# Performance work log

Measured on AMD Instinct MI355X. Metric: run time of the kernel, lower is better.

The kernel has to match this reference:

```python
import jax, jax.numpy as jnp
import numpy as np


def _topk_axis(x, k, axis, largest):
    # lax.top_k works on the last axis, largest, sorted descending.
    xm = jnp.moveaxis(x, axis, -1)
    if largest:
        vals, idx = jax.lax.top_k(xm, k)
    else:
        vals, idx = jax.lax.top_k(-xm, k)
        vals = -vals  # ascending smallest-k, matching torch.topk(largest=False, sorted=True)
    return jnp.moveaxis(vals, -1, axis), jnp.moveaxis(idx, -1, axis)


def setup_inputs() -> dict:
    key = jax.random.key(0)
    k0, k1, k2 = jax.random.split(key, 3)
    v_0 = jax.random.normal(k0, (4096, 32000), dtype=jnp.float32)
    v_1 = jax.random.normal(k1, (8, 16, 64, 4096), dtype=jnp.float32)
    v_2 = jax.random.normal(k2, (100000, 512), dtype=jnp.float32)
    return {"v_0": v_0, "v_1": v_1, "v_2": v_2}


def reference(v_0, v_1, v_2):
    # TopK_0: k=2, dim=1, largest, sorted
    v_4, v_5 = _topk_axis(v_0, 2, 1, largest=True)
    # TopK_1: k=4, dim=3, smallest, sorted
    v_7, v_8 = _topk_axis(v_1, 4, 3, largest=False)
    # TopK_2: k=3, dim=0, largest, sorted
    v_10, v_11 = _topk_axis(v_2, 3, 0, largest=True)
    return (v_4, v_5, v_7, v_8, v_10, v_11)
```

## Files before the change

kernel.cpp:

```cpp
#include <hip/hip_runtime.h>
#include <limits.h>
#include <math.h>

typedef unsigned long long u64;
typedef unsigned int u32;

__device__ __forceinline__ u32 f2ord(float v) {
    u32 u = __float_as_uint(v);
    return (u & 0x80000000u) ? ~u : (u | 0x80000000u);
}
__device__ __forceinline__ float ord2f(u32 s) {
    u32 u = (s & 0x80000000u) ? (s & 0x7FFFFFFFu) : ~s;
    return __uint_as_float(u);
}
__device__ __forceinline__ u64 keylg(float v, u32 i) { return ((u64)f2ord(v) << 32) | (u64)(~i); }
__device__ __forceinline__ u64 keysm(float v, u32 i) { return ((u64)f2ord(v) << 32) | (u64)i; }
__device__ __forceinline__ float val_of(u64 k) { return ord2f((u32)(k >> 32)); }
__device__ __forceinline__ float idxf_lg(u64 k) { return (float)(~(u32)k); }
__device__ __forceinline__ float idxf_sm(u64 k) { return (float)((u32)k); }

__device__ __forceinline__ u64 mx64(u64 a, u64 b) { return a > b ? a : b; }
__device__ __forceinline__ u64 mn64(u64 a, u64 b) { return a < b ? a : b; }

__device__ __forceinline__ void ins2_lg(u64& s0, u64& s1, u64 k) {
    u64 t0 = mx64(s0, k), r0 = mn64(s0, k);
    s0 = t0; s1 = mx64(s1, r0);
}
__device__ __forceinline__ void ins3_lg(u64& s0, u64& s1, u64& s2, u64 k) {
    u64 t0 = mx64(s0, k), r0 = mn64(s0, k);
    u64 t1 = mx64(s1, r0), r1 = mn64(s1, r0);
    s0 = t0; s1 = t1; s2 = mx64(s2, r1);
}
__device__ __forceinline__ void ins4_sm(u64& s0, u64& s1, u64& s2, u64& s3, u64 k) {
    u64 t0 = mn64(s0, k), r0 = mx64(s0, k);
    u64 t1 = mn64(s1, r0), r1 = mx64(s1, r0);
    u64 t2 = mn64(s2, r1), r2 = mx64(s2, r1);
    s0 = t0; s1 = t1; s2 = t2; s3 = mn64(s3, r2);
}

__device__ __forceinline__ void ce_max(u64& a, u64& b) { u64 h = mx64(a, b), l = mn64(a, b); a = h; b = l; }
__device__ __forceinline__ void ce_min(u64& a, u64& b) { u64 l = mn64(a, b), h = mx64(a, b); a = l; b = h; }

__device__ __forceinline__ void merge2_lg(u64& a0, u64& a1, u64 b0, u64 b1) {
    u64 l0 = mx64(a0, b1), l1 = mx64(a1, b0);
    a0 = mx64(l0, l1); a1 = mn64(l0, l1);
}
__device__ __forceinline__ void merge3_lg(u64& a0, u64& a1, u64& a2, u64 b0, u64 b1, u64 b2) {
    u64 l0 = mx64(a0, b2), l1 = mx64(a1, b1), l2 = mx64(a2, b0);
    ce_max(l0, l1); ce_max(l1, l2); ce_max(l0, l1);
    a0 = l0; a1 = l1; a2 = l2;
}
__device__ __forceinline__ void merge4_sm(u64& a0, u64& a1, u64& a2, u64& a3,
                                          u64 b0, u64 b1, u64 b2, u64 b3) {
    u64 l0 = mn64(a0, b3), l1 = mn64(a1, b2), l2 = mn64(a2, b1), l3 = mn64(a3, b0);
    ce_min(l0, l2); ce_min(l1, l3); ce_min(l0, l1); ce_min(l2, l3);
    a0 = l0; a1 = l1; a2 = l2; a3 = l3;
}

__device__ __forceinline__ u64 shx64(u64 v, int m) {
    u32 hi = __shfl_xor((u32)(v >> 32), m);
    u32 lo = __shfl_xor((u32)v, m);
    return ((u64)hi << 32) | (u64)lo;
}

__global__ __launch_bounds__(256) void mega_kernel(
    const float* __restrict__ x0, float* __restrict__ o0v, float* __restrict__ o0i,
    const float* __restrict__ x1, float* __restrict__ o1v, float* __restrict__ o1i,
    const float* __restrict__ x2, u64* __restrict__ part, int rpb)
{
    const int bid  = blockIdx.x;
    const int wave = threadIdx.x >> 6;
    const int lane = threadIdx.x & 63;

    if (bid < 1024) {
        const int row = bid * 4 + wave;
        const float4* xr = (const float4*)(x0 + (size_t)row * 32000);
        u64 s0 = 0, s1 = 0;

#define K0UPD(f, b) \
        ins2_lg(s0, s1, keylg((f).x, (u32)(b)));     \
        ins2_lg(s0, s1, keylg((f).y, (u32)(b) + 1)); \
        ins2_lg(s0, s1, keylg((f).z, (u32)(b) + 2)); \
        ins2_lg(s0, s1, keylg((f).w, (u32)(b) + 3))

        int v = lane;
        for (int it = 0; it < 31; ++it, v += 256) {
            float4 t0 = xr[v];
            float4 t1 = xr[v + 64];
            float4 t2 = xr[v + 128];
            float4 t3 = xr[v + 192];
            K0UPD(t0, v * 4); K0UPD(t1, (v + 64) * 4);
            K0UPD(t2, (v + 128) * 4); K0UPD(t3, (v + 192) * 4);
        }
        { float4 t = xr[v]; K0UPD(t, v * 4); }
#undef K0UPD

        for (int m = 1; m < 64; m <<= 1) {
            u64 b0 = shx64(s0, m), b1 = shx64(s1, m);
            merge2_lg(s0, s1, b0, b1);
        }
        if (lane == 0) {
            o0v[row * 2 + 0] = val_of(s0);  o0v[row * 2 + 1] = val_of(s1);
            o0i[row * 2 + 0] = idxf_lg(s0); o0i[row * 2 + 1] = idxf_lg(s1);
        }

    } else if (bid < 3072) {
        const int row = (bid - 1024) * 4 + wave;
        const float4* xr = (const float4*)(x1 + (size_t)row * 4096);
        u64 s0 = ~0ull, s1 = ~0ull, s2 = ~0ull, s3 = ~0ull;

#define K1UPD(f, b) \
        ins4_sm(s0, s1, s2, s3, keysm((f).x, (u32)(b)));     \
        ins4_sm(s0, s1, s2, s3, keysm((f).y, (u32)(b) + 1)); \
        ins4_sm(s0, s1, s2, s3, keysm((f).z, (u32)(b) + 2)); \
        ins4_sm(s0, s1, s2, s3, keysm((f).w, (u32)(b) + 3))

        int v = lane;
        for (int it = 0; it < 4; ++it, v += 256) {
            float4 t0 = xr[v];
            float4 t1 = xr[v + 64];
            float4 t2 = xr[v + 128];
            float4 t3 = xr[v + 192];
            K1UPD(t0, v * 4); K1UPD(t1, (v + 64) * 4);
            K1UPD(t2, (v + 128) * 4); K1UPD(t3, (v + 192) * 4);
        }
#undef K1UPD

        for (int m = 1; m < 64; m <<= 1) {
            u64 b0 = shx64(s0, m), b1 = shx64(s1, m);
            u64 b2 = shx64(s2, m), b3 = shx64(s3, m);
            merge4_sm(s0, s1, s2, s3, b0, b1, b2, b3);
        }
        if (lane == 0) {
            o1v[row * 4 + 0] = val_of(s0);  o1v[row * 4 + 1] = val_of(s1);
            o1v[row * 4 + 2] = val_of(s2);  o1v[row * 4 + 3] = val_of(s3);
            o1i[row * 4 + 0] = idxf_sm(s0); o1i[row * 4 + 1] = idxf_sm(s1);
            o1i[row * 4 + 2] = idxf_sm(s2); o1i[row * 4 + 3] = idxf_sm(s3);
        }

    } else {
        const int blk = bid - 3072;
        const int t   = threadIdx.x;
        const int h   = t >> 7;
        const int c0  = (t & 127) * 4;
        int rbeg = blk * rpb;
        int rend = rbeg + rpb; if (rend > 100000) rend = 100000;

        u64 a[4][3];
#pragma unroll
        for (int c = 0; c < 4; ++c) { a[c][0] = 0; a[c][1] = 0; a[c][2] = 0; }

#define P1LOAD(r) (*(const float4*)(x2 + (size_t)(r) * 512 + c0))
#define P1UPD(f, rr) \
        ins3_lg(a[0][0], a[0][1], a[0][2], keylg((f).x, (u32)(rr))); \
        ins3_lg(a[1][0], a[1][1], a[1][2], keylg((f).y, (u32)(rr))); \
        ins3_lg(a[2][0], a[2][1], a[2][2], keylg((f).z, (u32)(rr))); \
        ins3_lg(a[3][0], a[3][1], a[3][2], keylg((f).w, (u32)(rr)))

        int r = rbeg + h;
        for (; r + 6 < rend; r += 8) {
            float4 f0 = P1LOAD(r);
            float4 f1 = P1LOAD(r + 2);
            float4 f2 = P1LOAD(r + 4);
            float4 f3 = P1LOAD(r + 6);
            P1UPD(f0, r); P1UPD(f1, r + 2); P1UPD(f2, r + 4); P1UPD(f3, r + 6);
        }
        for (; r < rend; r += 2) {
            float4 f0 = P1LOAD(r);
            P1UPD(f0, r);
        }
#undef P1LOAD
#undef P1UPD

        const int p = blk * 2 + h;
        u64* base = part + (size_t)p * 3 * 512;
#pragma unroll
        for (int k = 0; k < 3; ++k)
#pragma unroll
            for (int c = 0; c < 4; ++c)
                base[k * 512 + c0 + c] = a[c][k];
    }
}

__global__ __launch_bounds__(256) void topk2_p2a(
    const u64* __restrict__ part, u64* __restrict__ part2)
{
    const int b = blockIdx.x;
    const int s = b >> 1, cb = b & 1;
    const int col = cb * 256 + threadIdx.x;

    u64 a0 = 0, a1 = 0, a2 = 0;
    const u64* base = part + (size_t)s * 8 * 1536;
#pragma unroll
    for (int p = 0; p < 8; ++p) {
        const u64* q = base + (size_t)p * 1536;
        u64 x0 = q[col], x1 = q[512 + col], x2 = q[1024 + col];
        merge3_lg(a0, a1, a2, x0, x1, x2);
    }
    part2[((size_t)s * 3 + 0) * 512 + col] = a0;
    part2[((size_t)s * 3 + 1) * 512 + col] = a1;
    part2[((size_t)s * 3 + 2) * 512 + col] = a2;
}

__global__ __launch_bounds__(256) void topk2_p2b(
    const u64* __restrict__ part2, float* __restrict__ outv, float* __restrict__ outi)
{
    const int wave = threadIdx.x >> 6;
    const int lane = threadIdx.x & 63;
    const int col  = blockIdx.x * 4 + wave;

    const u64* q0 = part2 + (size_t)lane * 1536 + col;
    const u64* q1 = part2 + (size_t)(lane + 64) * 1536 + col;
    u64 a0 = q0[0], a1 = q0[512], a2 = q0[1024];
    merge3_lg(a0, a1, a2, q1[0], q1[512], q1[1024]);

    for (int m = 1; m < 64; m <<= 1) {
        u64 b0 = shx64(a0, m), b1 = shx64(a1, m), b2 = shx64(a2, m);
        merge3_lg(a0, a1, a2, b0, b1, b2);
    }

    if (lane == 0) {
        outv[0 * 512 + col] = val_of(a0);
        outv[1 * 512 + col] = val_of(a1);
        outv[2 * 512 + col] = val_of(a2);
        outi[0 * 512 + col] = idxf_lg(a0);
        outi[1 * 512 + col] = idxf_lg(a1);
        outi[2 * 512 + col] = idxf_lg(a2);
    }
}

__global__ __launch_bounds__(256) void topk2_direct(
    const float* __restrict__ x, float* __restrict__ outv, float* __restrict__ outi)
{
    const int col = blockIdx.x * 256 + threadIdx.x;
    u64 a0 = 0, a1 = 0, a2 = 0;
    for (int r = 0; r < 100000; ++r) {
        float v = x[(size_t)r * 512 + col];
        ins3_lg(a0, a1, a2, keylg(v, (u32)r));
    }
    outv[0 * 512 + col] = val_of(a0);
    outv[1 * 512 + col] = val_of(a1);
    outv[2 * 512 + col] = val_of(a2);
    outi[0 * 512 + col] = idxf_lg(a0);
    outi[1 * 512 + col] = idxf_lg(a1);
    outi[2 * 512 + col] = idxf_lg(a2);
}

__global__ __launch_bounds__(256) void noop_kernel() {}

extern "C" void kernel_launch(void* const* d_in, const int* in_sizes, int n_in,
                              void* d_out, int out_size, void* d_ws, size_t ws_size,
                              hipStream_t stream) {
    const float* v0 = (const float*)d_in[0];
    const float* v1 = (const float*)d_in[1];
    const float* v2 = (const float*)d_in[2];
    float* out = (float*)d_out;

    float* o_v4  = out;
    float* o_v5  = out + 8192;
    float* o_v7  = out + 16384;
    float* o_v8  = out + 49152;
    float* o_v10 = out + 81920;
    float* o_v11 = out + 83456;

    const int NB = 512;
    int rpb = (100000 + NB - 1) / NB;
    if (rpb & 1) rpb++;
    size_t need = ((size_t)NB * 2 + 128) * 3 * 512 * sizeof(u64);

    if (ws_size >= need) {
        u64* part  = (u64*)d_ws;
        u64* part2 = part + (size_t)NB * 2 * 3 * 512;
        mega_kernel<<<3584, 256, 0, stream>>>(v0, o_v4, o_v5,
                                              v1, o_v7, o_v8,
                                              v2, part, rpb);
        topk2_p2a<<<256, 256, 0, stream>>>(part, part2);
        topk2_p2b<<<128, 256, 0, stream>>>(part2, o_v10, o_v11);
    } else {
        mega_kernel<<<3072, 256, 0, stream>>>(v0, o_v4, o_v5,
                                              v1, o_v7, o_v8,
                                              v2, (u64*)d_ws, 1 << 30);
        topk2_direct<<<2, 256, 0, stream>>>(v2, o_v10, o_v11);
    }
}
```

Measured before the change: 190.2 us.

## Schedule column-topk blocks first and collapse two-stage reduction into one kernel

The column-wise top-3 partial blocks move to the front of the mega-kernel grid, so the long per-column scans start early instead of running as a tail after the row top-k work. Each block now covers the full row chunk with two columns per thread rather than splitting rows across two halves. Only 512 partials are written, and a single reduce kernel merges 8 partials per lane, replacing the two-stage p2a/p2b reduction and saving a launch. The trade-off is longer serial chains per thread in the first phase and narrower float2 loads.

New measurement: 178.3 us. 1.07x faster.

```diff
diff --git a/kernel.cpp b/kernel.cpp
--- a/kernel.cpp
+++ b/kernel.cpp
@@ -66,14 +66,49 @@
 __global__ __launch_bounds__(256) void mega_kernel(
     const float* __restrict__ x0, float* __restrict__ o0v, float* __restrict__ o0i,
     const float* __restrict__ x1, float* __restrict__ o1v, float* __restrict__ o1i,
-    const float* __restrict__ x2, u64* __restrict__ part, int rpb)
+    const float* __restrict__ x2, u64* __restrict__ part, int rpb, int do_p1)
 {
     const int bid  = blockIdx.x;
     const int wave = threadIdx.x >> 6;
     const int lane = threadIdx.x & 63;
 
-    if (bid < 1024) {
-        const int row = bid * 4 + wave;
+    if (bid < 512) {
+        if (!do_p1) return;
+        const int blk = bid;
+        const int c0  = threadIdx.x * 2;
+        int rbeg = blk * rpb;
+        int rend = rbeg + rpb; if (rend > 100000) rend = 100000;
+
+        u64 a0 = 0, a1 = 0, a2 = 0;
+        u64 b0 = 0, b1 = 0, b2 = 0;
+
+#define P1LOAD(r) (*(const float2*)(x2 + (size_t)(r) * 512 + c0))
+#define P1UPD(f, rr) \
+        ins3_lg(a0, a1, a2, keylg((f).x, (u32)(rr))); \
+        ins3_lg(b0, b1, b2, keylg((f).y, (u32)(rr)))
+
+        int r = rbeg;
+        for (; r + 3 < rend; r += 4) {
+            float2 f0 = P1LOAD(r);
+            float2 f1 = P1LOAD(r + 1);
+            float2 f2 = P1LOAD(r + 2);
+            float2 f3 = P1LOAD(r + 3);
+            P1UPD(f0, r); P1UPD(f1, r + 1); P1UPD(f2, r + 2); P1UPD(f3, r + 3);
+        }
+        for (; r < rend; ++r) {
+            float2 f0 = P1LOAD(r);
+            P1UPD(f0, r);
+        }
+#undef P1LOAD
+#undef P1UPD
+
+        u64* base = part + (size_t)blk * 1536;
+        base[0 * 512 + c0] = a0; base[0 * 512 + c0 + 1] = b0;
+        base[1 * 512 + c0] = a1; base[1 * 512 + c0 + 1] = b1;
+        base[2 * 512 + c0] = a2; base[2 * 512 + c0 + 1] = b2;
+
+    } else if (bid < 1536) {
+        const int row = (bid - 512) * 4 + wave;
         const float4* xr = (const float4*)(x0 + (size_t)row * 32000);
         u64 s0 = 0, s1 = 0;
 
@@ -104,8 +139,8 @@
             o0i[row * 2 + 0] = idxf_lg(s0); o0i[row * 2 + 1] = idxf_lg(s1);
         }
 
-    } else if (bid < 3072) {
-        const int row = (bid - 1024) * 4 + wave;
+    } else {
+        const int row = (bid - 1536) * 4 + wave;
         const float4* xr = (const float4*)(x1 + (size_t)row * 4096);
         u64 s0 = ~0ull, s1 = ~0ull, s2 = ~0ull, s3 = ~0ull;
 
@@ -137,83 +172,22 @@
             o1i[row * 4 + 0] = idxf_sm(s0); o1i[row * 4 + 1] = idxf_sm(s1);
             o1i[row * 4 + 2] = idxf_sm(s2); o1i[row * 4 + 3] = idxf_sm(s3);
         }
-
-    } else {
-        const int blk = bid - 3072;
-        const int t   = threadIdx.x;
-        const int h   = t >> 7;
-        const int c0  = (t & 127) * 4;
-        int rbeg = blk * rpb;
-        int rend = rbeg + rpb; if (rend > 100000) rend = 100000;
-
-        u64 a[4][3];
-#pragma unroll
-        for (int c = 0; c < 4; ++c) { a[c][0] = 0; a[c][1] = 0; a[c][2] = 0; }
-
-#define P1LOAD(r) (*(const float4*)(x2 + (size_t)(r) * 512 + c0))
-#define P1UPD(f, rr) \
-        ins3_lg(a[0][0], a[0][1], a[0][2], keylg((f).x, (u32)(rr))); \
-        ins3_lg(a[1][0], a[1][1], a[1][2], keylg((f).y, (u32)(rr))); \
-        ins3_lg(a[2][0], a[2][1], a[2][2], keylg((f).z, (u32)(rr))); \
-        ins3_lg(a[3][0], a[3][1], a[3][2], keylg((f).w, (u32)(rr)))
-
-        int r = rbeg + h;
-        for (; r + 6 < rend; r += 8) {
-            float4 f0 = P1LOAD(r);
-            float4 f1 = P1LOAD(r + 2);
-            float4 f2 = P1LOAD(r + 4);
-            float4 f3 = P1LOAD(r + 6);
-            P1UPD(f0, r); P1UPD(f1, r + 2); P1UPD(f2, r + 4); P1UPD(f3, r + 6);
-        }
-        for (; r < rend; r += 2) {
-            float4 f0 = P1LOAD(r);
-            P1UPD(f0, r);
-        }
-#undef P1LOAD
-#undef P1UPD
-
-        const int p = blk * 2 + h;
-        u64* base = part + (size_t)p * 3 * 512;
-#pragma unroll
-        for (int k = 0; k < 3; ++k)
-#pragma unroll
-            for (int c = 0; c < 4; ++c)
-                base[k * 512 + c0 + c] = a[c][k];
-    }
-}
-
-__global__ __launch_bounds__(256) void topk2_p2a(
-    const u64* __restrict__ part, u64* __restrict__ part2)
-{
-    const int b = blockIdx.x;
-    const int s = b >> 1, cb = b & 1;
-    const int col = cb * 256 + threadIdx.x;
-
-    u64 a0 = 0, a1 = 0, a2 = 0;
-    const u64* base = part + (size_t)s * 8 * 1536;
-#pragma unroll
-    for (int p = 0; p < 8; ++p) {
-        const u64* q = base + (size_t)p * 1536;
-        u64 x0 = q[col], x1 = q[512 + col], x2 = q[1024 + col];
-        merge3_lg(a0, a1, a2, x0, x1, x2);
-    }
-    part2[((size_t)s * 3 + 0) * 512 + col] = a0;
-    part2[((size_t)s * 3 + 1) * 512 + col] = a1;
-    part2[((size_t)s * 3 + 2) * 512 + col] = a2;
-}
-
-__global__ __launch_bounds__(256) void topk2_p2b(
-    const u64* __restrict__ part2, float* __restrict__ outv, float* __restrict__ outi)
+    }
+}
+
+__global__ __launch_bounds__(256) void topk2_reduce(
+    const u64* __restrict__ part, float* __restrict__ outv, float* __restrict__ outi)
 {
     const int wave = threadIdx.x >> 6;
     const int lane = threadIdx.x & 63;
     const int col  = blockIdx.x * 4 + wave;
 
-    const u64* q0 = part2 + (size_t)lane * 1536 + col;
-    const u64* q1 = part2 + (size_t)(lane + 64) * 1536 + col;
-    u64 a0 = q0[0], a1 = q0[512], a2 = q0[1024];
-    merge3_lg(a0, a1, a2, q1[0], q1[512], q1[1024]);
-
+    u64 a0 = 0, a1 = 0, a2 = 0;
+#pragma unroll
+    for (int j = 0; j < 8; ++j) {
+        const u64* q = part + (size_t)(lane + 64 * j) * 1536 + col;
+        merge3_lg(a0, a1, a2, q[0], q[512], q[1024]);
+    }
     for (int m = 1; m < 64; m <<= 1) {
         u64 b0 = shx64(a0, m), b1 = shx64(a1, m), b2 = shx64(a2, m);
         merge3_lg(a0, a1, a2, b0, b1, b2);
@@ -246,8 +220,6 @@
     outi[2 * 512 + col] = idxf_lg(a2);
 }
 
-__global__ __launch_bounds__(256) void noop_kernel() {}
-
 extern "C" void kernel_launch(void* const* d_in, const int* in_sizes, int n_in,
                               void* d_out, int out_size, void* d_ws, size_t ws_size,
                               hipStream_t stream) {
@@ -265,21 +237,18 @@
 
     const int NB = 512;
     int rpb = (100000 + NB - 1) / NB;
-    if (rpb & 1) rpb++;
-    size_t need = ((size_t)NB * 2 + 128) * 3 * 512 * sizeof(u64);
+    size_t need = (size_t)NB * 3 * 512 * sizeof(u64);
 
     if (ws_size >= need) {
-        u64* part  = (u64*)d_ws;
-        u64* part2 = part + (size_t)NB * 2 * 3 * 512;
+        u64* part = (u64*)d_ws;
         mega_kernel<<<3584, 256, 0, stream>>>(v0, o_v4, o_v5,
                                               v1, o_v7, o_v8,
-                                              v2, part, rpb);
-        topk2_p2a<<<256, 256, 0, stream>>>(part, part2);
-        topk2_p2b<<<128, 256, 0, stream>>>(part2, o_v10, o_v11);
+                                              v2, part, rpb, 1);
+        topk2_reduce<<<128, 256, 0, stream>>>(part, o_v10, o_v11);
     } else {
-        mega_kernel<<<3072, 256, 0, stream>>>(v0, o_v4, o_v5,
+        mega_kernel<<<3584, 256, 0, stream>>>(v0, o_v4, o_v5,
                                               v1, o_v7, o_v8,
-                                              v2, (u64*)d_ws, 1 << 30);
+                                              v2, (u64*)d_ws, rpb, 0);
         topk2_direct<<<2, 256, 0, stream>>>(v2, o_v10, o_v11);
     }
 }
```
